# Optimization experiments

Hardware: AMD Instinct MI355X
Metric: run time of the kernel (lower is better)

## Reference

```python
import jax, jax.numpy as jnp
import numpy as np

B, T_PAST, T_FUT, IN, H = 512, 360, 1800, 3, 64
FUTURE_SEQ, WSPF = 50, 34


def _lstm_all_hidden(x, W_ih, W_hh, b_ih, b_hh):
    # x: [B, T, IN]; PyTorch LSTM, gate order i, f, g, o; returns h at every step [T, B, H]
    Hn = W_hh.shape[1]
    xg = jnp.einsum('bti,gi->btg', x, W_ih) + (b_ih + b_hh)  # [B, T, 4H]
    xg = jnp.swapaxes(xg, 0, 1)  # [T, B, 4H]

    def step(carry, g_x):
        h, c = carry
        gates = g_x + h @ W_hh.T  # [B, 4H]
        i = jax.nn.sigmoid(gates[:, 0 * Hn:1 * Hn])
        f = jax.nn.sigmoid(gates[:, 1 * Hn:2 * Hn])
        g = jnp.tanh(gates[:, 2 * Hn:3 * Hn])
        o = jax.nn.sigmoid(gates[:, 3 * Hn:4 * Hn])
        c = f * c + i * g
        h = o * jnp.tanh(c)
        return (h, c), h

    Bn = x.shape[0]
    init = (jnp.zeros((Bn, Hn), x.dtype), jnp.zeros((Bn, Hn), x.dtype))
    _, hs = jax.lax.scan(step, init, xg)
    return hs  # [T, B, H]


def setup_inputs() -> dict:
    key = jax.random.key(0)
    ks = jax.random.split(key, 8)
    s_ih = 1.0 / np.sqrt(H)
    return {
        'wave_input': jax.random.normal(ks[0], (B, T_PAST, IN), jnp.float32),
        'wave_future': jax.random.normal(ks[1], (B, T_FUT, IN), jnp.float32),
        'W_ih': jax.random.uniform(ks[2], (4 * H, IN), jnp.float32, -s_ih, s_ih),
        'W_hh': jax.random.uniform(ks[3], (4 * H, H), jnp.float32, -s_ih, s_ih),
        'b_ih': jax.random.uniform(ks[4], (4 * H,), jnp.float32, -s_ih, s_ih),
        'b_hh': jax.random.uniform(ks[5], (4 * H,), jnp.float32, -s_ih, s_ih),
        'W_proj': jax.random.uniform(ks[6], (H, H), jnp.float32, -s_ih, s_ih),
        'b_proj': jax.random.uniform(ks[7], (H,), jnp.float32, -s_ih, s_ih),
    }


def reference(wave_input, wave_future, W_ih, W_hh, b_ih, b_hh, W_proj, b_proj):
    # Original loop re-runs the LSTM from zero state over [past; future[:(t+1)*WSPF]].
    # Since every iteration's sequence is a prefix of the longest one, a single pass
    # over [past; future[:FUTURE_SEQ*WSPF]] yields identical hidden states; we just
    # gather h at times T_PAST + (t+1)*WSPF - 1.
    max_steps = FUTURE_SEQ * WSPF
    combined = jnp.concatenate([wave_input, wave_future[:, :max_steps, :]], axis=1)
    hs = _lstm_all_hidden(combined, W_ih, W_hh, b_ih, b_hh)  # [T, B, H]
    idx = T_PAST + (jnp.arange(FUTURE_SEQ) + 1) * WSPF - 1  # [F]
    ctx_h = hs[idx]  # [F, B, H]
    ctx = jnp.einsum('fbh,oh->fbo', ctx_h, W_proj) + b_proj  # Linear projection
    return jnp.swapaxes(ctx, 0, 1)  # [B, FUTURE_SEQ, H]
```

## Files before the change

### kernel.cpp

```cpp
#include <hip/hip_runtime.h>
#include <math.h>

#define BATCH     512
#define T_PAST_   360
#define T_FUT_    1800
#define IN_SZ     3
#define H_SZ      64
#define FUT_SEQ   50
#define WSPF_     34
#define MAX_STEPS (FUT_SEQ * WSPF_)
#define T_TOT     (T_PAST_ + MAX_STEPS)
#define NTHREADS  256

typedef __fp16 h2 __attribute__((ext_vector_type(2)));

__device__ __forceinline__ h2  as_h2(int v) { return __builtin_bit_cast(h2, v); }
__device__ __forceinline__ int as_i(h2 v)   { return __builtin_bit_cast(int, v); }
__device__ __forceinline__ float rcp_(float x) { return __builtin_amdgcn_rcpf(x); }

__device__ __forceinline__ float tanh_(float x) {
    float a = fabsf(x);
    float e = __expf(-2.0f * a);
    float t = (1.0f - e) * rcp_(1.0f + e);
    return copysignf(t, x);
}

__device__ __forceinline__ float dot2_(int a, int b, float c) {
#if __has_builtin(__builtin_amdgcn_fdot2)
    return __builtin_amdgcn_fdot2(as_h2(a), as_h2(b), c, false);
#else
    h2 av = as_h2(a), bv = as_h2(b);
    return fmaf((float)av.x, (float)bv.x, fmaf((float)av.y, (float)bv.y, c));
#endif
}

template <int PAT>
__device__ __forceinline__ float quadb_(float v) {
    return __builtin_bit_cast(float,
        __builtin_amdgcn_update_dpp(0, __builtin_bit_cast(int, v),
                                    PAT, 0xF, 0xF, true));
}

__device__ __forceinline__ float swz_xor4_(float v) {
    return __builtin_bit_cast(float,
        __builtin_amdgcn_ds_swizzle(__builtin_bit_cast(int, v), 0x101F));
}

__global__ __launch_bounds__(NTHREADS, 2)
void lstm_fused_kernel(const float* __restrict__ wave_input,
                       const float* __restrict__ wave_future,
                       const float* __restrict__ W_ih,
                       const float* __restrict__ W_hh,
                       const float* __restrict__ b_ih,
                       const float* __restrict__ b_hh,
                       const float* __restrict__ W_proj,
                       const float* __restrict__ b_proj,
                       float* __restrict__ out)
{
    __shared__ __align__(16) float x_lds[T_TOT * IN_SZ];
    __shared__ __align__(16) int   wp_lds[H_SZ * 33];
    __shared__ __align__(16) int   h2_lds[2][H_SZ / 2];

    const int b    = blockIdx.x;
    const int tid  = threadIdx.x;
    const int wv   = tid >> 6;
    const int lane = tid & 63;
    const int g    = lane & 3;
    const int u    = wv * 16 + (lane >> 2);
    const int row  = g * H_SZ + u;

    {
        const float* wi = wave_input + (size_t)b * (T_PAST_ * IN_SZ);
        for (int i = tid; i < T_PAST_ * IN_SZ; i += NTHREADS) x_lds[i] = wi[i];
        const float* wf = wave_future + (size_t)b * (T_FUT_ * IN_SZ);
        for (int i = tid; i < MAX_STEPS * IN_SZ; i += NTHREADS)
            x_lds[T_PAST_ * IN_SZ + i] = wf[i];
    }
    for (int i = tid; i < H_SZ * 32; i += NTHREADS) {
        int j = i >> 5, m = i & 31;
        wp_lds[j * 33 + m] = as_i(__builtin_amdgcn_cvt_pkrtz(
            W_proj[j * H_SZ + 2 * m], W_proj[j * H_SZ + 2 * m + 1]));
    }
    if (tid < 32) h2_lds[0][tid] = 0;

    const float scale = (g == 2) ? 2.0f : 1.0f;
    const float aa    = (g == 2) ? 2.0f : 1.0f;
    const float bb    = (g == 2) ? -1.0f : 0.0f;

    int w2[32];
    {
        const float* rowp = W_hh + (size_t)row * H_SZ;
        #pragma unroll
        for (int j = 0; j < 32; ++j)
            w2[j] = as_i(__builtin_amdgcn_cvt_pkrtz(rowp[2*j]   * scale,
                                                    rowp[2*j+1] * scale));
    }
    #pragma unroll
    for (int k = 0; k < 32; k += 8)
        asm volatile("" : "+v"(w2[k+0]), "+v"(w2[k+1]), "+v"(w2[k+2]), "+v"(w2[k+3]),
                          "+v"(w2[k+4]), "+v"(w2[k+5]), "+v"(w2[k+6]), "+v"(w2[k+7]));

    const float wih0 = W_ih[row * 3 + 0] * scale;
    const float wih1 = W_ih[row * 3 + 1] * scale;
    const float wih2 = W_ih[row * 3 + 2] * scale;
    const float bg   = (b_ih[row] + b_hh[row]) * scale;
    const float bpj  = b_proj[lane];

    float c = 0.0f;
    float* outb = out + (size_t)b * (FUT_SEQ * H_SZ);
    int next_cp = T_PAST_ + WSPF_ - 1;
    int cp_k = 0;

    __syncthreads();

    for (int t = 0; t < T_TOT; ++t) {
        const int4* hp4 = (const int4*)h2_lds[t & 1];
        float a0 = bg, a1 = 0.f, a2 = 0.f, a3 = 0.f;
        #pragma unroll
        for (int q = 0; q < 8; ++q) {
            int4 pv = hp4[q];
            a0 = dot2_(w2[4*q+0], pv.x, a0);
            a1 = dot2_(w2[4*q+1], pv.y, a1);
            a2 = dot2_(w2[4*q+2], pv.z, a2);
            a3 = dot2_(w2[4*q+3], pv.w, a3);
        }
        a1 = fmaf(wih0, x_lds[t*3+0], a1);
        a2 = fmaf(wih1, x_lds[t*3+1], a2);
        a3 = fmaf(wih2, x_lds[t*3+2], a3);
        float acc = (a0 + a1) + (a2 + a3);

        float e    = __expf(-acc);
        float gval = fmaf(aa, rcp_(1.0f + e), bb);

        float gi = quadb_<0x00>(gval);
        float gf = quadb_<0x55>(gval);
        float gg = quadb_<0xAA>(gval);
        float go = quadb_<0xFF>(gval);
        c = fmaf(gf, c, gi * gg);
        float h = go * tanh_(c);

        float hn = swz_xor4_(h);
        int pk = as_i(__builtin_amdgcn_cvt_pkrtz(h, hn));
        if ((lane & 7) == 0)
            h2_lds[(t + 1) & 1][wv * 8 + (lane >> 3)] = pk;
        __syncthreads();

        if (t == next_cp) {
            const int4* ph4 = (const int4*)h2_lds[(t + 1) & 1];
            float p = bpj;
            #pragma unroll
            for (int q = 0; q < 8; ++q) {
                int4 pv = ph4[q];
                p = dot2_(wp_lds[lane * 33 + 4*q+0], pv.x, p);
                p = dot2_(wp_lds[lane * 33 + 4*q+1], pv.y, p);
                p = dot2_(wp_lds[lane * 33 + 4*q+2], pv.z, p);
                p = dot2_(wp_lds[lane * 33 + 4*q+3], pv.w, p);
            }
            if (wv == 0) outb[cp_k * H_SZ + lane] = p;
            next_cp += WSPF_;
            ++cp_k;
        }
    }
}

extern "C" void kernel_launch(void* const* d_in, const int* in_sizes, int n_in,
                              void* d_out, int out_size, void* d_ws, size_t ws_size,
                              hipStream_t stream) {
    const float* wave_input  = (const float*)d_in[0];
    const float* wave_future = (const float*)d_in[1];
    const float* W_ih        = (const float*)d_in[2];
    const float* W_hh        = (const float*)d_in[3];
    const float* b_ih        = (const float*)d_in[4];
    const float* b_hh        = (const float*)d_in[5];
    const float* W_proj      = (const float*)d_in[6];
    const float* b_proj      = (const float*)d_in[7];
    float* out               = (float*)d_out;

    lstm_fused_kernel<<<BATCH, NTHREADS, 0, stream>>>(
        wave_input, wave_future, W_ih, W_hh, b_ih, b_hh, W_proj, b_proj, out);
}
```

Before: 833.0 us.

## Process two batch elements per block to amortize recurrence sync latency

Each block now runs two independent LSTM sequences (b and b+256), interleaving their dot products and activations so the per-step barrier and LDS latency are shared across twice the work. The launch drops to 256 blocks, which matches roughly one block per CU. It also switches to exp2 with the log2e factor folded into the weights and packs the inputs to fp16 for dot2. Checkpoint hidden states are stashed in LDS and projected after the loop, which takes the projection off the serial critical path. In exchange, register pressure rises and half as many blocks are available to hide latency.

```diff
diff --git a/kernel.cpp b/kernel.cpp
--- a/kernel.cpp
+++ b/kernel.cpp
@@ -2,6 +2,7 @@
 #include <math.h>
 
 #define BATCH     512
+#define NBLK      256
 #define T_PAST_   360
 #define T_FUT_    1800
 #define IN_SZ     3
@@ -11,6 +12,7 @@
 #define MAX_STEPS (FUT_SEQ * WSPF_)
 #define T_TOT     (T_PAST_ + MAX_STEPS)
 #define NTHREADS  256
+#define LOG2E     1.44269504f
 
 typedef __fp16 h2 __attribute__((ext_vector_type(2)));
 
@@ -18,9 +20,17 @@
 __device__ __forceinline__ int as_i(h2 v)   { return __builtin_bit_cast(int, v); }
 __device__ __forceinline__ float rcp_(float x) { return __builtin_amdgcn_rcpf(x); }
 
-__device__ __forceinline__ float tanh_(float x) {
+__device__ __forceinline__ float exp2_(float x) {
+#if __has_builtin(__builtin_amdgcn_exp2f)
+    return __builtin_amdgcn_exp2f(x);
+#else
+    return exp2f(x);
+#endif
+}
+
+__device__ __forceinline__ float tanh2_(float x) {
     float a = fabsf(x);
-    float e = __expf(-2.0f * a);
+    float e = exp2_(a * -2.885390082f);
     float t = (1.0f - e) * rcp_(1.0f + e);
     return copysignf(t, x);
 }
@@ -39,11 +49,6 @@
     return __builtin_bit_cast(float,
         __builtin_amdgcn_update_dpp(0, __builtin_bit_cast(int, v),
                                     PAT, 0xF, 0xF, true));
-}
-
-__device__ __forceinline__ float swz_xor4_(float v) {
-    return __builtin_bit_cast(float,
-        __builtin_amdgcn_ds_swizzle(__builtin_bit_cast(int, v), 0x101F));
 }
 
 __global__ __launch_bounds__(NTHREADS, 2)
@@ -57,9 +62,10 @@
                        const float* __restrict__ b_proj,
                        float* __restrict__ out)
 {
-    __shared__ __align__(16) float x_lds[T_TOT * IN_SZ];
-    __shared__ __align__(16) int   wp_lds[H_SZ * 33];
-    __shared__ __align__(16) int   h2_lds[2][H_SZ / 2];
+    __shared__ __align__(16) int    x2_lds[2][T_TOT * 2];
+    __shared__ __align__(16) int    wp_lds[H_SZ * 33];
+    __shared__ __align__(16) __fp16 h2buf[2][2][H_SZ];
+    __shared__ __align__(16) __fp16 stash[2][FUT_SEQ][H_SZ];
 
     const int b    = blockIdx.x;
     const int tid  = threadIdx.x;
@@ -70,20 +76,32 @@
     const int row  = g * H_SZ + u;
 
     {
-        const float* wi = wave_input + (size_t)b * (T_PAST_ * IN_SZ);
-        for (int i = tid; i < T_PAST_ * IN_SZ; i += NTHREADS) x_lds[i] = wi[i];
-        const float* wf = wave_future + (size_t)b * (T_FUT_ * IN_SZ);
-        for (int i = tid; i < MAX_STEPS * IN_SZ; i += NTHREADS)
-            x_lds[T_PAST_ * IN_SZ + i] = wf[i];
+        const float* wiA = wave_input  + (size_t)b * (T_PAST_ * IN_SZ);
+        const float* wiB = wave_input  + (size_t)(b + NBLK) * (T_PAST_ * IN_SZ);
+        for (int i = tid; i < T_PAST_; i += NTHREADS) {
+            x2_lds[0][2*i  ] = as_i(__builtin_amdgcn_cvt_pkrtz(wiA[3*i], wiA[3*i+1]));
+            x2_lds[0][2*i+1] = as_i(__builtin_amdgcn_cvt_pkrtz(wiA[3*i+2], 0.0f));
+            x2_lds[1][2*i  ] = as_i(__builtin_amdgcn_cvt_pkrtz(wiB[3*i], wiB[3*i+1]));
+            x2_lds[1][2*i+1] = as_i(__builtin_amdgcn_cvt_pkrtz(wiB[3*i+2], 0.0f));
+        }
+        const float* wfA = wave_future + (size_t)b * (T_FUT_ * IN_SZ);
+        const float* wfB = wave_future + (size_t)(b + NBLK) * (T_FUT_ * IN_SZ);
+        for (int i = tid; i < MAX_STEPS; i += NTHREADS) {
+            int tt = T_PAST_ + i;
+            x2_lds[0][2*tt  ] = as_i(__builtin_amdgcn_cvt_pkrtz(wfA[3*i], wfA[3*i+1]));
+            x2_lds[0][2*tt+1] = as_i(__builtin_amdgcn_cvt_pkrtz(wfA[3*i+2], 0.0f));
+            x2_lds[1][2*tt  ] = as_i(__builtin_amdgcn_cvt_pkrtz(wfB[3*i], wfB[3*i+1]));
+            x2_lds[1][2*tt+1] = as_i(__builtin_amdgcn_cvt_pkrtz(wfB[3*i+2], 0.0f));
+        }
     }
     for (int i = tid; i < H_SZ * 32; i += NTHREADS) {
         int j = i >> 5, m = i & 31;
         wp_lds[j * 33 + m] = as_i(__builtin_amdgcn_cvt_pkrtz(
             W_proj[j * H_SZ + 2 * m], W_proj[j * H_SZ + 2 * m + 1]));
     }
-    if (tid < 32) h2_lds[0][tid] = 0;
-
-    const float scale = (g == 2) ? 2.0f : 1.0f;
+    if (tid < 2 * H_SZ) h2buf[tid >> 6][0][tid & 63] = (__fp16)0.0f;
+
+    const float scale = ((g == 2) ? 2.0f : 1.0f) * LOG2E;
     const float aa    = (g == 2) ? 2.0f : 1.0f;
     const float bb    = (g == 2) ? -1.0f : 0.0f;
 
@@ -100,66 +118,82 @@
         asm volatile("" : "+v"(w2[k+0]), "+v"(w2[k+1]), "+v"(w2[k+2]), "+v"(w2[k+3]),
                           "+v"(w2[k+4]), "+v"(w2[k+5]), "+v"(w2[k+6]), "+v"(w2[k+7]));
 
-    const float wih0 = W_ih[row * 3 + 0] * scale;
-    const float wih1 = W_ih[row * 3 + 1] * scale;
-    const float wih2 = W_ih[row * 3 + 2] * scale;
-    const float bg   = (b_ih[row] + b_hh[row]) * scale;
-    const float bpj  = b_proj[lane];
-
-    float c = 0.0f;
-    float* outb = out + (size_t)b * (FUT_SEQ * H_SZ);
+    const int wi01 = as_i(__builtin_amdgcn_cvt_pkrtz(W_ih[row*3+0] * scale,
+                                                     W_ih[row*3+1] * scale));
+    const int wi2p = as_i(__builtin_amdgcn_cvt_pkrtz(W_ih[row*3+2] * scale, 0.0f));
+    const float bg = (b_ih[row] + b_hh[row]) * scale;
+
+    float cA = 0.0f, cB = 0.0f;
     int next_cp = T_PAST_ + WSPF_ - 1;
     int cp_k = 0;
 
     __syncthreads();
 
     for (int t = 0; t < T_TOT; ++t) {
-        const int4* hp4 = (const int4*)h2_lds[t & 1];
-        float a0 = bg, a1 = 0.f, a2 = 0.f, a3 = 0.f;
+        const int4* hA4 = (const int4*)h2buf[0][t & 1];
+        const int4* hB4 = (const int4*)h2buf[1][t & 1];
+        float aA0 = bg, aA1 = 0.f, aA2 = 0.f, aA3 = 0.f;
+        float aB0 = bg, aB1 = 0.f, aB2 = 0.f, aB3 = 0.f;
         #pragma unroll
         for (int q = 0; q < 8; ++q) {
-            int4 pv = hp4[q];
-            a0 = dot2_(w2[4*q+0], pv.x, a0);
-            a1 = dot2_(w2[4*q+1], pv.y, a1);
-            a2 = dot2_(w2[4*q+2], pv.z, a2);
-            a3 = dot2_(w2[4*q+3], pv.w, a3);
-        }
-        a1 = fmaf(wih0, x_lds[t*3+0], a1);
-        a2 = fmaf(wih1, x_lds[t*3+1], a2);
-        a3 = fmaf(wih2, x_lds[t*3+2], a3);
-        float acc = (a0 + a1) + (a2 + a3);
-
-        float e    = __expf(-acc);
-        float gval = fmaf(aa, rcp_(1.0f + e), bb);
-
-        float gi = quadb_<0x00>(gval);
-        float gf = quadb_<0x55>(gval);
-        float gg = quadb_<0xAA>(gval);
-        float go = quadb_<0xFF>(gval);
-        c = fmaf(gf, c, gi * gg);
-        float h = go * tanh_(c);
-
-        float hn = swz_xor4_(h);
-        int pk = as_i(__builtin_amdgcn_cvt_pkrtz(h, hn));
-        if ((lane & 7) == 0)
-            h2_lds[(t + 1) & 1][wv * 8 + (lane >> 3)] = pk;
+            int4 pv = hA4[q];
+            aA0 = dot2_(w2[4*q+0], pv.x, aA0);
+            aA1 = dot2_(w2[4*q+1], pv.y, aA1);
+            aA2 = dot2_(w2[4*q+2], pv.z, aA2);
+            aA3 = dot2_(w2[4*q+3], pv.w, aA3);
+        }
+        #pragma unroll
+        for (int q = 0; q < 8; ++q) {
+            int4 pv = hB4[q];
+            aB0 = dot2_(w2[4*q+0], pv.x, aB0);
+            aB1 = dot2_(w2[4*q+1], pv.y, aB1);
+            aB2 = dot2_(w2[4*q+2], pv.z, aB2);
+            aB3 = dot2_(w2[4*q+3], pv.w, aB3);
+        }
+        aA1 = dot2_(wi01, x2_lds[0][2*t], aA1);
+        aA2 = dot2_(wi2p, x2_lds[0][2*t+1], aA2);
+        aB1 = dot2_(wi01, x2_lds[1][2*t], aB1);
+        aB2 = dot2_(wi2p, x2_lds[1][2*t+1], aB2);
+        float accA = (aA0 + aA1) + (aA2 + aA3);
+        float accB = (aB0 + aB1) + (aB2 + aB3);
+
+        float gvA = fmaf(aa, rcp_(1.0f + exp2_(-accA)), bb);
+        float gvB = fmaf(aa, rcp_(1.0f + exp2_(-accB)), bb);
+
+        float giA = quadb_<0x00>(gvA), gfA = quadb_<0x55>(gvA);
+        float ggA = quadb_<0xAA>(gvA), goA = quadb_<0xFF>(gvA);
+        float giB = quadb_<0x00>(gvB), gfB = quadb_<0x55>(gvB);
+        float ggB = quadb_<0xAA>(gvB), goB = quadb_<0xFF>(gvB);
+        cA = fmaf(gfA, cA, giA * ggA);
+        cB = fmaf(gfB, cB, giB * ggB);
+        float hA = goA * tanh2_(cA);
+        float hB = goB * tanh2_(cB);
+
+        if (g == 0) {
+            h2buf[0][(t + 1) & 1][u] = (__fp16)hA;
+            h2buf[1][(t + 1) & 1][u] = (__fp16)hB;
+        }
         __syncthreads();
 
         if (t == next_cp) {
-            const int4* ph4 = (const int4*)h2_lds[(t + 1) & 1];
-            float p = bpj;
-            #pragma unroll
-            for (int q = 0; q < 8; ++q) {
-                int4 pv = ph4[q];
-                p = dot2_(wp_lds[lane * 33 + 4*q+0], pv.x, p);
-                p = dot2_(wp_lds[lane * 33 + 4*q+1], pv.y, p);
-                p = dot2_(wp_lds[lane * 33 + 4*q+2], pv.z, p);
-                p = dot2_(wp_lds[lane * 33 + 4*q+3], pv.w, p);
-            }
-            if (wv == 0) outb[cp_k * H_SZ + lane] = p;
+            if (tid < 2 * H_SZ)
+                stash[tid >> 6][cp_k][tid & 63] = h2buf[tid >> 6][(t + 1) & 1][tid & 63];
             next_cp += WSPF_;
             ++cp_k;
         }
+    }
+
+    __syncthreads();
+    for (int idx = tid; idx < 2 * FUT_SEQ * H_SZ; idx += NTHREADS) {
+        int e = (idx >= FUT_SEQ * H_SZ);
+        int r = idx - e * (FUT_SEQ * H_SZ);
+        int k = r >> 6, j = r & 63;
+        const int* hs = (const int*)&stash[e][k][0];
+        float p = b_proj[j];
+        #pragma unroll 8
+        for (int m = 0; m < 32; ++m)
+            p = dot2_(wp_lds[j * 33 + m], hs[m], p);
+        out[((size_t)(e ? b + NBLK : b) * FUT_SEQ + k) * H_SZ + j] = p;
     }
 }
 
@@ -176,6 +210,6 @@
     const float* b_proj      = (const float*)d_in[7];
     float* out               = (float*)d_out;
 
-    lstm_fused_kernel<<<BATCH, NTHREADS, 0, stream>>>(
+    lstm_fused_kernel<<<NBLK, NTHREADS, 0, stream>>>(
         wave_input, wave_future, W_ih, W_hh, b_ih, b_hh, W_proj, b_proj, out);
 }
```

Result: slower. 943.4 us (+13.2%).

## Split LSTM recurrence dot product across two threads per gate row; defer projection

Applied to the files above, without the earlier changes.

Doubles the block to 512 threads so each gate row's 64-wide recurrent dot product is split across two lanes, with a swizzle adding the two halves. This halves the serial dot-product chain per step. The inputs are packed to fp16 and folded in with dot2, and LOG2E is folded into the weights so exp2 is used directly. The checkpoint projections are stashed and computed after the loop, taking the branchy projection out of the recurrence. The cost is one extra cross-lane exchange per step, a barrier over twice as many threads, and fp16 rounding of the inputs.

```diff
diff --git a/kernel.cpp b/kernel.cpp
--- a/kernel.cpp
+++ b/kernel.cpp
@@ -10,7 +10,8 @@
 #define WSPF_     34
 #define MAX_STEPS (FUT_SEQ * WSPF_)
 #define T_TOT     (T_PAST_ + MAX_STEPS)
-#define NTHREADS  256
+#define NTHREADS  512
+#define LOG2E     1.44269504f
 
 typedef __fp16 h2 __attribute__((ext_vector_type(2)));
 
@@ -18,9 +19,17 @@
 __device__ __forceinline__ int as_i(h2 v)   { return __builtin_bit_cast(int, v); }
 __device__ __forceinline__ float rcp_(float x) { return __builtin_amdgcn_rcpf(x); }
 
-__device__ __forceinline__ float tanh_(float x) {
+__device__ __forceinline__ float exp2_(float x) {
+#if __has_builtin(__builtin_amdgcn_exp2f)
+    return __builtin_amdgcn_exp2f(x);
+#else
+    return exp2f(x);
+#endif
+}
+
+__device__ __forceinline__ float tanh2_(float x) {
     float a = fabsf(x);
-    float e = __expf(-2.0f * a);
+    float e = exp2_(a * -2.885390082f);
     float t = (1.0f - e) * rcp_(1.0f + e);
     return copysignf(t, x);
 }
@@ -57,109 +66,113 @@
                        const float* __restrict__ b_proj,
                        float* __restrict__ out)
 {
-    __shared__ __align__(16) float x_lds[T_TOT * IN_SZ];
-    __shared__ __align__(16) int   wp_lds[H_SZ * 33];
-    __shared__ __align__(16) int   h2_lds[2][H_SZ / 2];
+    __shared__ __align__(16) int    x2_lds[T_TOT * 2];
+    __shared__ __align__(16) int    wp_lds[H_SZ * 33];
+    __shared__ __align__(16) __fp16 h2buf[2][H_SZ];
+    __shared__ __align__(16) __fp16 stash[FUT_SEQ][H_SZ];
 
     const int b    = blockIdx.x;
     const int tid  = threadIdx.x;
     const int wv   = tid >> 6;
     const int lane = tid & 63;
     const int g    = lane & 3;
-    const int u    = wv * 16 + (lane >> 2);
+    const int kh   = (lane >> 2) & 1;
+    const int u    = wv * 8 + (lane >> 3);
     const int row  = g * H_SZ + u;
 
     {
         const float* wi = wave_input + (size_t)b * (T_PAST_ * IN_SZ);
-        for (int i = tid; i < T_PAST_ * IN_SZ; i += NTHREADS) x_lds[i] = wi[i];
+        for (int i = tid; i < T_PAST_; i += NTHREADS) {
+            x2_lds[2*i  ] = as_i(__builtin_amdgcn_cvt_pkrtz(wi[3*i], wi[3*i+1]));
+            x2_lds[2*i+1] = as_i(__builtin_amdgcn_cvt_pkrtz(wi[3*i+2], 0.0f));
+        }
         const float* wf = wave_future + (size_t)b * (T_FUT_ * IN_SZ);
-        for (int i = tid; i < MAX_STEPS * IN_SZ; i += NTHREADS)
-            x_lds[T_PAST_ * IN_SZ + i] = wf[i];
+        for (int i = tid; i < MAX_STEPS; i += NTHREADS) {
+            int tt = T_PAST_ + i;
+            x2_lds[2*tt  ] = as_i(__builtin_amdgcn_cvt_pkrtz(wf[3*i], wf[3*i+1]));
+            x2_lds[2*tt+1] = as_i(__builtin_amdgcn_cvt_pkrtz(wf[3*i+2], 0.0f));
+        }
     }
     for (int i = tid; i < H_SZ * 32; i += NTHREADS) {
         int j = i >> 5, m = i & 31;
         wp_lds[j * 33 + m] = as_i(__builtin_amdgcn_cvt_pkrtz(
             W_proj[j * H_SZ + 2 * m], W_proj[j * H_SZ + 2 * m + 1]));
     }
-    if (tid < 32) h2_lds[0][tid] = 0;
+    if (tid < H_SZ) h2buf[0][tid] = (__fp16)0.0f;
 
-    const float scale = (g == 2) ? 2.0f : 1.0f;
+    const float scale = ((g == 2) ? 2.0f : 1.0f) * LOG2E;
     const float aa    = (g == 2) ? 2.0f : 1.0f;
     const float bb    = (g == 2) ? -1.0f : 0.0f;
 
-    int w2[32];
+    int w2[16];
     {
-        const float* rowp = W_hh + (size_t)row * H_SZ;
+        const float* rowp = W_hh + (size_t)row * H_SZ + kh * 32;
         #pragma unroll
-        for (int j = 0; j < 32; ++j)
+        for (int j = 0; j < 16; ++j)
             w2[j] = as_i(__builtin_amdgcn_cvt_pkrtz(rowp[2*j]   * scale,
                                                     rowp[2*j+1] * scale));
     }
     #pragma unroll
-    for (int k = 0; k < 32; k += 8)
+    for (int k = 0; k < 16; k += 8)
         asm volatile("" : "+v"(w2[k+0]), "+v"(w2[k+1]), "+v"(w2[k+2]), "+v"(w2[k+3]),
                           "+v"(w2[k+4]), "+v"(w2[k+5]), "+v"(w2[k+6]), "+v"(w2[k+7]));
 
-    const float wih0 = W_ih[row * 3 + 0] * scale;
-    const float wih1 = W_ih[row * 3 + 1] * scale;
-    const float wih2 = W_ih[row * 3 + 2] * scale;
-    const float bg   = (b_ih[row] + b_hh[row]) * scale;
-    const float bpj  = b_proj[lane];
+    const int wi01 = (kh == 0)
+        ? as_i(__builtin_amdgcn_cvt_pkrtz(W_ih[row*3+0] * scale, W_ih[row*3+1] * scale))
+        : 0;
+    const int wi2p = (kh == 0)
+        ? as_i(__builtin_amdgcn_cvt_pkrtz(W_ih[row*3+2] * scale, 0.0f))
+        : 0;
+    const float bgl = (kh == 0) ? (b_ih[row] + b_hh[row]) * scale : 0.0f;
 
     float c = 0.0f;
-    float* outb = out + (size_t)b * (FUT_SEQ * H_SZ);
     int next_cp = T_PAST_ + WSPF_ - 1;
     int cp_k = 0;
 
     __syncthreads();
 
     for (int t = 0; t < T_TOT; ++t) {
-        const int4* hp4 = (const int4*)h2_lds[t & 1];
-        float a0 = bg, a1 = 0.f, a2 = 0.f, a3 = 0.f;
-        #pragma unroll
-        for (int q = 0; q < 8; ++q) {
-            int4 pv = hp4[q];
-            a0 = dot2_(w2[4*q+0], pv.x, a0);
-            a1 = dot2_(w2[4*q+1], pv.y, a1);
-            a2 = dot2_(w2[4*q+2], pv.z, a2);
-            a3 = dot2_(w2[4*q+3], pv.w, a3);
-        }
-        a1 = fmaf(wih0, x_lds[t*3+0], a1);
-        a2 = fmaf(wih1, x_lds[t*3+1], a2);
-        a3 = fmaf(wih2, x_lds[t*3+2], a3);
-        float acc = (a0 + a1) + (a2 + a3);
+        const int4* hp4 = (const int4*)&h2buf[t & 1][kh * 32];
+        int4 p0 = hp4[0], p1 = hp4[1], p2 = hp4[2], p3 = hp4[3];
+        float a0 = bgl, a1 = 0.f, a2 = 0.f, a3 = 0.f;
+        a0 = dot2_(w2[ 0], p0.x, a0); a1 = dot2_(w2[ 1], p0.y, a1);
+        a2 = dot2_(w2[ 2], p0.z, a2); a3 = dot2_(w2[ 3], p0.w, a3);
+        a0 = dot2_(w2[ 4], p1.x, a0); a1 = dot2_(w2[ 5], p1.y, a1);
+        a2 = dot2_(w2[ 6], p1.z, a2); a3 = dot2_(w2[ 7], p1.w, a3);
+        a0 = dot2_(w2[ 8], p2.x, a0); a1 = dot2_(w2[ 9], p2.y, a1);
+        a2 = dot2_(w2[10], p2.z, a2); a3 = dot2_(w2[11], p2.w, a3);
+        a0 = dot2_(w2[12], p3.x, a0); a1 = dot2_(w2[13], p3.y, a1);
+        a2 = dot2_(w2[14], p3.z, a2); a3 = dot2_(w2[15], p3.w, a3);
+        a1 = dot2_(wi01, x2_lds[2*t],   a1);
+        a2 = dot2_(wi2p, x2_lds[2*t+1], a2);
+        float half = (a0 + a1) + (a2 + a3);
 
-        float e    = __expf(-acc);
-        float gval = fmaf(aa, rcp_(1.0f + e), bb);
+        float acc = half + swz_xor4_(half);
+        float gval = fmaf(aa, rcp_(1.0f + exp2_(-acc)), bb);
 
         float gi = quadb_<0x00>(gval);
         float gf = quadb_<0x55>(gval);
         float gg = quadb_<0xAA>(gval);
         float go = quadb_<0xFF>(gval);
         c = fmaf(gf, c, gi * gg);
-        float h = go * tanh_(c);
+        float h = go * tanh2_(c);
 
-        float hn = swz_xor4_(h);
-        int pk = as_i(__builtin_amdgcn_cvt_pkrtz(h, hn));
-        if ((lane & 7) == 0)
-            h2_lds[(t + 1) & 1][wv * 8 + (lane >> 3)] = pk;
+        if ((lane & 7) == 0) {
+            h2buf[(t + 1) & 1][u] = (__fp16)h;
+            if (t == next_cp) stash[cp_k][u] = (__fp16)h;
+        }
+        if (t == next_cp) { next_cp += WSPF_; ++cp_k; }
         __syncthreads();
+    }
 
-        if (t == next_cp) {
-            const int4* ph4 = (const int4*)h2_lds[(t + 1) & 1];
-            float p = bpj;
-            #pragma unroll
-            for (int q = 0; q < 8; ++q) {
-                int4 pv = ph4[q];
-                p = dot2_(wp_lds[lane * 33 + 4*q+0], pv.x, p);
-                p = dot2_(wp_lds[lane * 33 + 4*q+1], pv.y, p);
-                p = dot2_(wp_lds[lane * 33 + 4*q+2], pv.z, p);
-                p = dot2_(wp_lds[lane * 33 + 4*q+3], pv.w, p);
-            }
-            if (wv == 0) outb[cp_k * H_SZ + lane] = p;
-            next_cp += WSPF_;
-            ++cp_k;
-        }
+    for (int idx = tid; idx < FUT_SEQ * H_SZ; idx += NTHREADS) {
+        int k = idx >> 6, j = idx & 63;
+        const int* hs = (const int*)&stash[k][0];
+        float p = b_proj[j];
+        #pragma unroll 8
+        for (int m = 0; m < 32; ++m)
+            p = dot2_(wp_lds[j * 33 + m], hs[m], p);
+        out[((size_t)b * FUT_SEQ + k) * H_SZ + j] = p;
     }
 }
 
```

Result: slower. 973.5 us (+16.9%).
